# Kernel optimization log

Measured on AMD Instinct MI355X. Metric: run time of the kernel, lower is better.

Reference implementation:

```python
import jax, jax.numpy as jnp
import numpy as np


def _pool_masks(corners, size):
    # Reproduce torch: corners/4; LL=clamp(LL,0,21); UR=clamp(where(UR-LL>=2,UR,LL+2),2,23);
    # then int() truncation (== floor for nonneg) of both bounds before slicing.
    c = corners / 4.0
    LL = jnp.clip(c[:, :, 0, :], 0.0, 21.0)            # [B,P,3]
    UR = c[:, :, 1, :]
    UR = jnp.clip(jnp.where(UR - LL >= 2.0, UR, LL + 2.0), 2.0, 23.0)
    lo = jnp.floor(LL).astype(jnp.int32)               # [B,P,3]
    n = jnp.floor(UR).astype(jnp.int32) - lo           # crop length per axis, >= 2
    # AdaptiveMaxPool3d(output_size=2) bins: bin k covers [floor(k*n/2), ceil((k+1)*n/2))
    k = jnp.arange(2)
    bin_lo = lo[:, :, None, :] + (k[None, None, :, None] * n[:, :, None, :]) // 2            # [B,P,2,3]
    bin_hi = lo[:, :, None, :] + ((k[None, None, :, None] + 1) * n[:, :, None, :] + 1) // 2  # [B,P,2,3]
    idx = jnp.arange(size)
    # per-axis boolean membership masks, each [B,P,2,size]
    return [(idx >= bin_lo[:, :, :, a, None]) & (idx < bin_hi[:, :, :, a, None]) for a in range(3)]


def reference(fm, corners):
    # fm: [B,C,D,H,W] with D=H=W=24; corners: [B,P,2,3] float voxel coords
    B, C, D, H, W = fm.shape
    mx, my, mz = _pool_masks(corners, D)
    neg = jnp.asarray(-jnp.inf, fm.dtype)
    # Adaptive max-pool over a separable box == nested per-axis masked maxes (fused by XLA under jit).
    # axis x: [B,P,C,2,H,W]
    t = jnp.where(mx[:, :, None, :, :, None, None], fm[:, None, :, None, :, :, :], neg).max(axis=4)
    # axis y: [B,P,C,2,2,W]
    t = jnp.where(my[:, :, None, None, :, :, None], t[:, :, :, :, None, :, :], neg).max(axis=5)
    # axis z: [B,P,C,2,2,2]
    t = jnp.where(mz[:, :, None, None, None, :, :], t[:, :, :, :, :, None, :], neg).max(axis=6)
    return t


def setup_inputs() -> dict:
    key = jax.random.key(0)
    k1, k2 = jax.random.split(key)
    fm = jax.random.normal(k1, (4, 64, 24, 24, 24), dtype=jnp.float32)
    # raw corner coords in original-volume voxels [0, 96); module divides by 4 internally
    corners = jax.random.uniform(k2, (4, 64, 2, 3), dtype=jnp.float32) * 96.0
    return {"fm": fm, "corners": corners}
```

## Files before the change

### kernel.cpp

```cpp
#include <hip/hip_runtime.h>
#include <math.h>


#define FM_CH 13824

__global__ __launch_bounds__(64) void crop_pool_kernel(
    const float* __restrict__ fm,
    const float* __restrict__ corners,
    float* __restrict__ out)
{
    const int idx  = blockIdx.x;
    const int c    = idx & 63;
    const int bn   = idx >> 6;
    const int b    = bn >> 6;
    const int lane = threadIdx.x;
    const int bin  = lane >> 3;
    const int sub  = lane & 7;
    const int kx = (bin >> 2) & 1;
    const int ky = (bin >> 1) & 1;
    const int kz =  bin       & 1;

    int lo[3], nn[3];
#pragma unroll
    for (int a = 0; a < 3; ++a) {
        float LL = corners[bn * 6 + a] * 0.25f;
        LL = fminf(fmaxf(LL, 0.0f), 21.0f);
        float UR = corners[bn * 6 + 3 + a] * 0.25f;
        UR = (UR - LL >= 2.0f) ? UR : (LL + 2.0f);
        UR = fminf(fmaxf(UR, 2.0f), 23.0f);
        lo[a] = (int)floorf(LL);
        nn[a] = (int)floorf(UR) - lo[a];
    }

    const int ks[3] = {kx, ky, kz};
    int s0[3], s1[3];
#pragma unroll
    for (int a = 0; a < 3; ++a) {
        s0[a] = lo[a] + ((ks[a] * nn[a]) >> 1);
        s1[a] = lo[a] + (((ks[a] + 1) * nn[a] + 1) >> 1);
    }
    const int ny  = s1[1] - s0[1];
    const int nz  = s1[2] - s0[2];
    const int vol = (s1[0] - s0[0]) * ny * nz;

    const float* fmb = fm + (size_t)(b * 64 + c) * FM_CH;

    float m = -INFINITY;
    for (int i = sub; i < vol; i += 8) {
        int z = i % nz;
        int t = i / nz;
        int y = t % ny;
        int x = t / ny;
        m = fmaxf(m, fmb[((s0[0] + x) * 24 + (s0[1] + y)) * 24 + (s0[2] + z)]);
    }

#pragma unroll
    for (int off = 1; off < 8; off <<= 1)
        m = fmaxf(m, __shfl_xor(m, off));

    if (sub == 0)
        out[idx * 8 + bin] = m;
}

extern "C" void kernel_launch(void* const* d_in, const int* in_sizes, int n_in,
                              void* d_out, int out_size, void* d_ws, size_t ws_size,
                              hipStream_t stream)
{
    const float* fm      = (const float*)d_in[0];
    const float* corners = (const float*)d_in[1];
    float* out           = (float*)d_out;

    crop_pool_kernel<<<16384, 64, 0, stream>>>(fm, corners, out);
}
```

Measured before the change: 71.35 us.

## Reorder work so consecutive waves share a channel, use magic-number division and unroll

Each 64-lane wave still handles one (batch, box, channel) triple, but waves are now ordered box-fastest, so concurrently running waves read the same feature-map channel and get more L2 reuse. Four waves are packed per 256-thread block. Integer div/mod is replaced by multiply-shift reciprocals, and the gather loop is unrolled into four independent max accumulators to raise memory-level parallelism. Output writes are gathered via a shuffle so that eight lanes store contiguous bins.

```diff
diff --git a/kernel.cpp b/kernel.cpp
--- a/kernel.cpp
+++ b/kernel.cpp
@@ -4,23 +4,23 @@
 
 #define FM_CH 13824
 
-__global__ __launch_bounds__(64) void crop_pool_kernel(
+__global__ __launch_bounds__(256) void crop_pool_kernel(
     const float* __restrict__ fm,
     const float* __restrict__ corners,
     float* __restrict__ out)
 {
-    const int idx  = blockIdx.x;
-    const int c    = idx & 63;
-    const int bn   = idx >> 6;
-    const int b    = bn >> 6;
-    const int lane = threadIdx.x;
-    const int bin  = lane >> 3;
-    const int sub  = lane & 7;
-    const int kx = (bin >> 2) & 1;
-    const int ky = (bin >> 1) & 1;
-    const int kz =  bin       & 1;
+    const int lane = threadIdx.x & 63;
+    const int w    = blockIdx.x * 4 + (threadIdx.x >> 6);
+    const int n = w & 63;
+    const int c = (w >> 6) & 63;
+    const int b = w >> 12;
+    const int bn = b * 64 + n;
 
-    int lo[3], nn[3];
+    const int bin = lane >> 3;
+    const int sub = lane & 7;
+    const int ks[3] = { (bin >> 2) & 1, (bin >> 1) & 1, bin & 1 };
+
+    int s0[3], s1[3];
 #pragma unroll
     for (int a = 0; a < 3; ++a) {
         float LL = corners[bn * 6 + a] * 0.25f;
@@ -28,38 +28,48 @@
         float UR = corners[bn * 6 + 3 + a] * 0.25f;
         UR = (UR - LL >= 2.0f) ? UR : (LL + 2.0f);
         UR = fminf(fmaxf(UR, 2.0f), 23.0f);
-        lo[a] = (int)floorf(LL);
-        nn[a] = (int)floorf(UR) - lo[a];
+        int lo = (int)floorf(LL);
+        int nn = (int)floorf(UR) - lo;
+        s0[a] = lo + ((ks[a] * nn) >> 1);
+        s1[a] = lo + (((ks[a] + 1) * nn + 1) >> 1);
     }
+    const unsigned ny  = (unsigned)(s1[1] - s0[1]);
+    const unsigned nz  = (unsigned)(s1[2] - s0[2]);
+    const unsigned vol = (unsigned)(s1[0] - s0[0]) * ny * nz;
 
-    const int ks[3] = {kx, ky, kz};
-    int s0[3], s1[3];
-#pragma unroll
-    for (int a = 0; a < 3; ++a) {
-        s0[a] = lo[a] + ((ks[a] * nn[a]) >> 1);
-        s1[a] = lo[a] + (((ks[a] + 1) * nn[a] + 1) >> 1);
+    const unsigned Mz = (1u << 19) / nz + 1;
+    const unsigned My = (1u << 19) / ny + 1;
+
+    const float* base = fm + (size_t)(b * 64 + c) * FM_CH
+                           + ((s0[0] * 24 + s0[1]) * 24 + s0[2]);
+
+    auto voxel = [&](unsigned i) -> float {
+        unsigned q = (i * Mz) >> 19;
+        unsigned z = i - q * nz;
+        unsigned x = (q * My) >> 19;
+        unsigned y = q - x * ny;
+        return base[x * 576u + y * 24u + z];
+    };
+
+    float m0 = -INFINITY, m1 = -INFINITY, m2 = -INFINITY, m3 = -INFINITY;
+    unsigned i = sub;
+    for (; i + 24 < vol; i += 32) {
+        m0 = fmaxf(m0, voxel(i));
+        m1 = fmaxf(m1, voxel(i + 8));
+        m2 = fmaxf(m2, voxel(i + 16));
+        m3 = fmaxf(m3, voxel(i + 24));
     }
-    const int ny  = s1[1] - s0[1];
-    const int nz  = s1[2] - s0[2];
-    const int vol = (s1[0] - s0[0]) * ny * nz;
-
-    const float* fmb = fm + (size_t)(b * 64 + c) * FM_CH;
-
-    float m = -INFINITY;
-    for (int i = sub; i < vol; i += 8) {
-        int z = i % nz;
-        int t = i / nz;
-        int y = t % ny;
-        int x = t / ny;
-        m = fmaxf(m, fmb[((s0[0] + x) * 24 + (s0[1] + y)) * 24 + (s0[2] + z)]);
-    }
+    for (; i < vol; i += 8)
+        m0 = fmaxf(m0, voxel(i));
+    float m = fmaxf(fmaxf(m0, m1), fmaxf(m2, m3));
 
 #pragma unroll
     for (int off = 1; off < 8; off <<= 1)
         m = fmaxf(m, __shfl_xor(m, off));
 
-    if (sub == 0)
-        out[idx * 8 + bin] = m;
+    float v = __shfl(m, (lane & 7) << 3);
+    if (lane < 8)
+        out[((size_t)(bn * 64 + c)) * 8 + lane] = v;
 }
 
 extern "C" void kernel_launch(void* const* d_in, const int* in_sizes, int n_in,
@@ -70,5 +80,5 @@
     const float* corners = (const float*)d_in[1];
     float* out           = (float*)d_out;
 
-    crop_pool_kernel<<<16384, 64, 0, stream>>>(fm, corners, out);
+    crop_pool_kernel<<<4096, 256, 0, stream>>>(fm, corners, out);
 }
```

After: 69.94 us. 1.02x faster.

## Transpose feature map to channels-last and pool with vectorized channel loads

Applied to the files above, without the earlier changes.

Adds a shared-memory transpose kernel that rewrites the feature map from [B,C,S] to [B,S,C] in workspace. The pool kernel then gives each wavefront one (box, bin) task and has lanes read contiguous float4 channel groups, which removes the strided per-channel gathers and integer div/mod indexing. The cost is an extra full pass over the feature map (read plus write, about 14 MB) and a second launch. Run time then depends on whether the coalesced box reads outweigh that transpose traffic.

```diff
diff --git a/kernel.cpp b/kernel.cpp
--- a/kernel.cpp
+++ b/kernel.cpp
@@ -2,25 +2,52 @@
 #include <math.h>
 
 
-#define FM_CH 13824
+#define SPAT 13824
 
-__global__ __launch_bounds__(64) void crop_pool_kernel(
-    const float* __restrict__ fm,
-    const float* __restrict__ corners,
+__global__ __launch_bounds__(256) void transpose_kernel(
+    const float* __restrict__ fm, float* __restrict__ ws)
+{
+    __shared__ float tile[64][65];
+    const int b  = blockIdx.y;
+    const int s0 = blockIdx.x * 64;
+    const int t  = threadIdx.x;
+    const int sl = t & 63;
+    const int r0 = t >> 6;
+
+    const float* src = fm + (size_t)b * 64 * SPAT;
+#pragma unroll
+    for (int p = 0; p < 16; ++p) {
+        const int cl = r0 * 16 + p;
+        tile[cl][sl] = src[(size_t)cl * SPAT + s0 + sl];
+    }
+    __syncthreads();
+    float* dst = ws + ((size_t)b * SPAT + s0) * 64;
+#pragma unroll
+    for (int p = 0; p < 16; ++p) {
+        const int srow = r0 * 16 + p;
+        dst[(size_t)srow * 64 + sl] = tile[sl][srow];
+    }
+}
+
+__device__ __forceinline__ float4 fmax4(float4 a, float4 b) {
+    return make_float4(fmaxf(a.x, b.x), fmaxf(a.y, b.y),
+                       fmaxf(a.z, b.z), fmaxf(a.w, b.w));
+}
+
+__global__ __launch_bounds__(256) void pool_kernel(
+    const float* __restrict__ corners, const float* __restrict__ ws,
     float* __restrict__ out)
 {
-    const int idx  = blockIdx.x;
-    const int c    = idx & 63;
-    const int bn   = idx >> 6;
+    const int task = blockIdx.x * 4 + (threadIdx.x >> 6);
+    const int bin  = task & 7;
+    const int bn   = task >> 3;
     const int b    = bn >> 6;
-    const int lane = threadIdx.x;
-    const int bin  = lane >> 3;
-    const int sub  = lane & 7;
-    const int kx = (bin >> 2) & 1;
-    const int ky = (bin >> 1) & 1;
-    const int kz =  bin       & 1;
+    const int lane = threadIdx.x & 63;
+    const int cg   = lane >> 4;
+    const int cq   = lane & 15;
+    const int ks[3] = { (bin >> 2) & 1, (bin >> 1) & 1, bin & 1 };
 
-    int lo[3], nn[3];
+    int s0a[3], s1a[3];
 #pragma unroll
     for (int a = 0; a < 3; ++a) {
         float LL = corners[bn * 6 + a] * 0.25f;
@@ -28,38 +55,40 @@
         float UR = corners[bn * 6 + 3 + a] * 0.25f;
         UR = (UR - LL >= 2.0f) ? UR : (LL + 2.0f);
         UR = fminf(fmaxf(UR, 2.0f), 23.0f);
-        lo[a] = (int)floorf(LL);
-        nn[a] = (int)floorf(UR) - lo[a];
+        const int lo = (int)floorf(LL);
+        const int nn = (int)floorf(UR) - lo;
+        s0a[a] = lo + ((ks[a] * nn) >> 1);
+        s1a[a] = lo + (((ks[a] + 1) * nn + 1) >> 1);
     }
 
-    const int ks[3] = {kx, ky, kz};
-    int s0[3], s1[3];
-#pragma unroll
-    for (int a = 0; a < 3; ++a) {
-        s0[a] = lo[a] + ((ks[a] * nn[a]) >> 1);
-        s1[a] = lo[a] + (((ks[a] + 1) * nn[a] + 1) >> 1);
-    }
-    const int ny  = s1[1] - s0[1];
-    const int nz  = s1[2] - s0[2];
-    const int vol = (s1[0] - s0[0]) * ny * nz;
+    const float4* base = (const float4*)(ws) + (size_t)b * SPAT * 16 + cq;
 
-    const float* fmb = fm + (size_t)(b * 64 + c) * FM_CH;
-
-    float m = -INFINITY;
-    for (int i = sub; i < vol; i += 8) {
-        int z = i % nz;
-        int t = i / nz;
-        int y = t % ny;
-        int x = t / ny;
-        m = fmaxf(m, fmb[((s0[0] + x) * 24 + (s0[1] + y)) * 24 + (s0[2] + z)]);
+    float4 m = make_float4(-INFINITY, -INFINITY, -INFINITY, -INFINITY);
+    for (int x = s0a[0]; x < s1a[0]; ++x) {
+        const int rx = x * 576;
+        for (int y = s0a[1]; y < s1a[1]; ++y) {
+            const int srow = rx + y * 24;
+            for (int z = s0a[2] + cg; z < s1a[2]; z += 4) {
+                m = fmax4(m, base[(size_t)(srow + z) * 16]);
+            }
+        }
     }
 
 #pragma unroll
-    for (int off = 1; off < 8; off <<= 1)
-        m = fmaxf(m, __shfl_xor(m, off));
+    for (int off = 16; off < 64; off <<= 1) {
+        m.x = fmaxf(m.x, __shfl_xor(m.x, off));
+        m.y = fmaxf(m.y, __shfl_xor(m.y, off));
+        m.z = fmaxf(m.z, __shfl_xor(m.z, off));
+        m.w = fmaxf(m.w, __shfl_xor(m.w, off));
+    }
 
-    if (sub == 0)
-        out[idx * 8 + bin] = m;
+    if (lane < 16) {
+        float* o = out + ((size_t)bn * 64 + 4 * cq) * 8 + bin;
+        o[0]  = m.x;
+        o[8]  = m.y;
+        o[16] = m.z;
+        o[24] = m.w;
+    }
 }
 
 extern "C" void kernel_launch(void* const* d_in, const int* in_sizes, int n_in,
@@ -69,6 +98,10 @@
     const float* fm      = (const float*)d_in[0];
     const float* corners = (const float*)d_in[1];
     float* out           = (float*)d_out;
+    float* ws            = (float*)d_ws;
 
-    crop_pool_kernel<<<16384, 64, 0, stream>>>(fm, corners, out);
+    dim3 tgrid(SPAT / 64, 4);
+    transpose_kernel<<<tgrid, 256, 0, stream>>>(fm, ws);
+
+    pool_kernel<<<512, 256, 0, stream>>>(corners, ws, out);
 }
```

Result: slower. 99.53 us (+39.5%).
